# Kernel optimization log

Hardware: AMD Instinct MI355X
Metric: run time of the kernel (lower is better)

## Reference

```python
import jax, jax.numpy as jnp
import numpy as np

# dims chosen per input_specs / init_kwargs
B, S, D_IN, UNITS, WIN = 4, 2048, 512, 64, 32
W = 2 * WIN + 1  # max window length


def setup_inputs() -> dict:
    key = jax.random.key(0)
    ks = jax.random.split(key, 8)
    p = lambda k, shape: jax.random.normal(k, shape, dtype=jnp.float32) * 0.02
    return {
        "query": jax.random.normal(ks[0], (B, S, D_IN), dtype=jnp.float32),
        "value": jax.random.normal(ks[1], (B, S, D_IN), dtype=jnp.float32),
        "Wq": p(ks[2], (D_IN, UNITS)), "bq": jnp.zeros((UNITS,), jnp.float32),
        "Wk": p(ks[3], (D_IN, UNITS)), "bk": jnp.zeros((UNITS,), jnp.float32),
        "Wv": p(ks[4], (D_IN, UNITS)), "bv": jnp.zeros((UNITS,), jnp.float32),
    }


def reference(query, value, Wq, bq, Wk, bk, Wv, bv):
    # Dense projections (query stream -> Q, value stream -> K and V)
    Q = query @ Wq + bq
    K = value @ Wk + bk
    V = value @ Wv + bv

    i = np.arange(S)
    start = np.maximum(i - WIN, 0)            # [S]
    end = np.minimum(i + WIN + 1, S)          # [S]
    lengths = end - start                      # [S] window length per position
    offsets = np.concatenate([[0], np.cumsum(lengths)[:-1]])
    L = int(lengths.sum())                     # total output seq length (concat of all windows)

    idx = start[:, None] + np.arange(W)[None, :]   # [S, W] window token indices
    valid = idx < end[:, None]                      # [S, W] which slots exist
    idx_c = np.minimum(idx, S - 1)                  # clamp for safe gather

    idx_c = jnp.asarray(idx_c)
    valid_j = jnp.asarray(valid)

    # Gather overlapping windows: [B, S, W, UNITS]
    Ql = Q[:, idx_c]
    Kl = K[:, idx_c]
    Vl = V[:, idx_c]

    # Faithful to original: ALL window rows act as queries for window i.
    scale = 1.0 / jnp.sqrt(jnp.asarray(UNITS, dtype=Q.dtype))
    scores = jnp.einsum("bswd,bsud->bswu", Ql, Kl) * scale  # [B, S, W, W]
    neg = jnp.finfo(scores.dtype).min
    scores = jnp.where(valid_j[None, :, None, :], scores, neg)  # mask padded keys
    weights = jax.nn.softmax(scores, axis=-1)
    out_local = jnp.einsum("bswu,bsud->bswd", weights, Vl)  # [B, S, W, UNITS]

    # Concat valid rows of every window along seq axis -> [B, L, UNITS]
    flat_pos = jnp.asarray(offsets)[:, None] + jnp.arange(W)[None, :]  # [S, W]
    flat_pos = jnp.where(valid_j, flat_pos, L)  # invalid rows dumped in slot L
    out = jnp.zeros((Q.shape[0], L + 1, UNITS), dtype=out_local.dtype)
    out = out.at[:, flat_pos.reshape(-1)].set(out_local.reshape(Q.shape[0], -1, UNITS))
    return out[:, :L]
```

## Files before the change

kernel.cpp:

```cpp
#include <hip/hip_runtime.h>
#include <hip/hip_bf16.h>

#define BB 4
#define SS 2048
#define DIN 512
#define UU 64
#define WINR 32
#define LTOT 132064
#define GQ 16
#define NWP 144
#define KST 66

typedef __attribute__((ext_vector_type(8))) short short8;
typedef __attribute__((ext_vector_type(4))) float float4v;

static __device__ __forceinline__ ushort f2bf(float f) {
    union { __hip_bfloat16 h; ushort u; } c;
    c.h = __float2bfloat16(f);
    return c.u;
}
static __device__ __forceinline__ float bf2f(ushort u) {
    union { float f; uint v; } c;
    c.v = ((uint)u) << 16;
    return c.f;
}

__device__ __forceinline__ int offs_of(int s) {
    int a = s < (SS - 33) ? s : (SS - 33);
    int m = (s - 33) > 0 ? (s - 33) : 0;
    return a * (a - 1) / 2 + 33 * a + (s - a) * SS - m * (m + 1) / 2;
}

__global__ __launch_bounds__(256) void prep_w(
    const float* __restrict__ Wq, const float* __restrict__ Wk, const float* __restrict__ Wv,
    ushort* __restrict__ Wt)
{
    __shared__ float T[64][65];
    const int mtx = blockIdx.x >> 3;
    const int kc  = blockIdx.x & 7;
    const float* W = (mtx == 0) ? Wq : ((mtx == 1) ? Wk : Wv);
    const int tid = threadIdx.x;
    for (int idx = tid; idx < 64 * 64; idx += 256) {
        const int k = idx >> 6, n = idx & 63;
        T[n][k] = W[(size_t)(kc * 64 + k) * UU + n];
    }
    __syncthreads();
    for (int idx = tid; idx < 64 * 64; idx += 256) {
        const int n = idx >> 6, kl = idx & 63;
        Wt[(size_t)mtx * UU * DIN + (size_t)n * DIN + kc * 64 + kl] = f2bf(T[n][kl]);
    }
}

__global__ __launch_bounds__(256) void qkv_mfma(
    const float* __restrict__ query, const float* __restrict__ value,
    const ushort* __restrict__ Wt,
    const float* __restrict__ bq, const float* __restrict__ bk, const float* __restrict__ bv,
    float* __restrict__ Qs, ushort* __restrict__ Kf, ushort* __restrict__ Vf)
{
    __shared__ float red[4][16 * UU];
    const int bid = blockIdx.x;
    const int mtx = bid >> 9;
    const int rt  = bid & 511;
    const int tid = threadIdx.x;
    const int kq = tid >> 6;
    const int lane = tid & 63;
    const int m16 = lane & 15, quad = lane >> 4;

    const float* X = (mtx == 0) ? query : value;
    const float* Xrow = X + (size_t)(rt * 16 + m16) * DIN + kq * 128 + quad * 8;
    const ushort* Wm = Wt + (size_t)mtx * UU * DIN + (size_t)m16 * DIN + kq * 128 + quad * 8;

    float4v acc[4];
#pragma unroll
    for (int nb = 0; nb < 4; ++nb) acc[nb] = (float4v){0.f, 0.f, 0.f, 0.f};

#pragma unroll
    for (int kk = 0; kk < 4; ++kk) {
        const float4 xa = *(const float4*)(Xrow + kk * 32);
        const float4 xb = *(const float4*)(Xrow + kk * 32 + 4);
        short8 a;
        a[0] = (short)f2bf(xa.x); a[1] = (short)f2bf(xa.y);
        a[2] = (short)f2bf(xa.z); a[3] = (short)f2bf(xa.w);
        a[4] = (short)f2bf(xb.x); a[5] = (short)f2bf(xb.y);
        a[6] = (short)f2bf(xb.z); a[7] = (short)f2bf(xb.w);
#pragma unroll
        for (int nb = 0; nb < 4; ++nb) {
            const short8 bfr = *(const short8*)(Wm + (size_t)nb * 16 * DIN + kk * 32);
            acc[nb] = __builtin_amdgcn_mfma_f32_16x16x32_bf16(a, bfr, acc[nb], 0, 0, 0);
        }
    }

#pragma unroll
    for (int nb = 0; nb < 4; ++nb)
#pragma unroll
        for (int reg = 0; reg < 4; ++reg)
            red[kq][(quad * 4 + reg) * UU + nb * 16 + m16] = acc[nb][reg];
    __syncthreads();

    const float* bias = (mtx == 0) ? bq : ((mtx == 1) ? bk : bv);
#pragma unroll
    for (int i = 0; i < 4; ++i) {
        const int e = tid + 256 * i;
        const int col = e & 63, row = e >> 6;
        float s = red[0][e] + red[1][e] + red[2][e] + red[3][e] + bias[col];
        const size_t gi = (size_t)(rt * 16 + row) * UU + col;
        if (mtx == 0)      Qs[gi] = s * 0.125f;
        else if (mtx == 1) Kf[gi] = f2bf(s);
        else               Vf[gi] = f2bf(s);
    }
}

__global__ __launch_bounds__(1024) void attn_kernel(
    const float* __restrict__ Qs, const ushort* __restrict__ Kf,
    const ushort* __restrict__ Vf, float* __restrict__ out)
{
    __shared__ ushort Kl[NWP * KST];
    __shared__ ushort Vl[NWP * KST];
    __shared__ float  ev[GQ][NWP];
    __shared__ float  qr[GQ][UU];

    const int blk = blockIdx.x;
    const int b = blk >> 7;
    const int q0 = (blk & 127) << 4;
    const int tid = threadIdx.x;

    const int j0 = max(q0 - 2 * WINR, 0);
    const int j1 = min(q0 + GQ - 1 + 2 * WINR + 1, SS);
    const int nw = j1 - j0;

    if (tid < GQ * UU)
        qr[tid >> 6][tid & 63] = Qs[((size_t)b * SS + q0) * UU + tid];

    const uint* Kg = (const uint*)(Kf + ((size_t)b * SS + j0) * UU);
    const uint* Vg = (const uint*)(Vf + ((size_t)b * SS + j0) * UU);
    for (int idx = tid; idx < nw * 32; idx += 1024) {
        const int j = idx >> 5, d2 = idx & 31;
        ((uint*)(Kl + j * KST))[d2] = Kg[idx];
        ((uint*)(Vl + j * KST))[d2] = Vg[idx];
    }
    __syncthreads();

    for (int item = tid; item < GQ * NWP; item += 1024) {
        const int g = item / NWP, jj = item - g * NWP;
        float e = 0.f;
        if (jj < nw) {
            const uint* kr = (const uint*)(Kl + jj * KST);
            const float* q = qr[g];
            float dot = 0.f;
#pragma unroll
            for (int p = 0; p < UU / 2; ++p) {
                const uint kp = kr[p];
                dot = fmaf(q[2 * p],     bf2f((ushort)kp),         dot);
                dot = fmaf(q[2 * p + 1], bf2f((ushort)(kp >> 16)), dot);
            }
            e = __expf(dot);
        }
        ev[g][jj] = e;
    }
    __syncthreads();

    const int w = tid >> 6, lane = tid & 63;
    const int qi = q0 + w;
    const int s_lo = max(qi - WINR, 0);
    const int s_hi = min(qi + WINR, SS - 1);
    int st = max(s_lo - WINR, 0);
    int en = min(s_lo + WINR + 1, SS);
    const float* evg = ev[w];

    float acc = 0.f, den = 0.f;
    for (int j = st; j < en; ++j) {
        const float e = evg[j - j0];
        acc = fmaf(e, bf2f(Vl[(j - j0) * KST + lane]), acc);
        den += e;
    }
    int off = offs_of(s_lo);
    float* outb = out + (size_t)b * LTOT * UU;
    for (int s = s_lo;; ++s) {
        outb[(size_t)(off + qi - st) * UU + lane] = acc * __builtin_amdgcn_rcpf(den);
        if (s == s_hi) break;
        off += en - st;
        if (en < SS) {
            const float e = evg[en - j0];
            acc = fmaf(e, bf2f(Vl[(en - j0) * KST + lane]), acc);
            den += e;
            ++en;
        }
        if (s + 1 > WINR) {
            const float e = evg[st - j0];
            acc = fmaf(-e, bf2f(Vl[(st - j0) * KST + lane]), acc);
            den -= e;
            ++st;
        }
    }
}

extern "C" void kernel_launch(void* const* d_in, const int* in_sizes, int n_in,
                              void* d_out, int out_size, void* d_ws, size_t ws_size,
                              hipStream_t stream) {
    const float* query = (const float*)d_in[0];
    const float* value = (const float*)d_in[1];
    const float* Wq = (const float*)d_in[2];
    const float* bq = (const float*)d_in[3];
    const float* Wk = (const float*)d_in[4];
    const float* bk = (const float*)d_in[5];
    const float* Wv = (const float*)d_in[6];
    const float* bv = (const float*)d_in[7];
    float* out = (float*)d_out;

    float* Qs = (float*)d_ws;
    ushort* Kf = (ushort*)(Qs + (size_t)BB * SS * UU);
    ushort* Vf = Kf + (size_t)BB * SS * UU;
    ushort* Wt = (ushort*)((float*)d_out + (size_t)out_size) - (size_t)3 * UU * DIN;

    prep_w<<<24, 256, 0, stream>>>(Wq, Wk, Wv, Wt);
    qkv_mfma<<<3 * 512, 256, 0, stream>>>(query, value, Wt, bq, bk, bv, Qs, Kf, Vf);
    attn_kernel<<<512, 1024, 0, stream>>>(Qs, Kf, Vf, out);
}
```

Before: 210.5 us.

## Transpose V in LDS, compute per-query scores from global K, vectorize sliding window

The attention kernel now stores V transposed and zero-padded in LDS, so each lane reads contiguous V values with 128-bit loads. K is no longer staged: each wavefront computes scores for its own query straight from global K, masking non-window keys to zero. The running window sum is split into separate add and remove accumulators processed eight at a time with vector loads. This cuts LDS traffic and scalar per-step loads, but adds redundant global K reads and an extra zeroing pass, and subtracting the two accumulators may change float rounding.

```diff
diff --git a/kernel.cpp b/kernel.cpp
--- a/kernel.cpp
+++ b/kernel.cpp
@@ -8,11 +8,11 @@
 #define WINR 32
 #define LTOT 132064
 #define GQ 16
-#define NWP 144
-#define KST 66
+#define VST 200
 
 typedef __attribute__((ext_vector_type(8))) short short8;
 typedef __attribute__((ext_vector_type(4))) float float4v;
+typedef __attribute__((ext_vector_type(4))) uint uint4v;
 
 static __device__ __forceinline__ ushort f2bf(float f) {
     union { __hip_bfloat16 h; ushort u; } c;
@@ -22,6 +22,11 @@
 static __device__ __forceinline__ float bf2f(ushort u) {
     union { float f; uint v; } c;
     c.v = ((uint)u) << 16;
+    return c.f;
+}
+static __device__ __forceinline__ float bfbits(uint u) {
+    union { float f; uint v; } c;
+    c.v = u;
     return c.f;
 }
 
@@ -114,83 +119,133 @@
     const float* __restrict__ Qs, const ushort* __restrict__ Kf,
     const ushort* __restrict__ Vf, float* __restrict__ out)
 {
-    __shared__ ushort Kl[NWP * KST];
-    __shared__ ushort Vl[NWP * KST];
-    __shared__ float  ev[GQ][NWP];
-    __shared__ float  qr[GQ][UU];
+    __shared__ ushort Vt[UU * VST];
+    __shared__ float  evf[GQ * VST];
 
     const int blk = blockIdx.x;
     const int b = blk >> 7;
     const int q0 = (blk & 127) << 4;
     const int tid = threadIdx.x;
+    const int lane = tid & 63;
+    const int wq = __builtin_amdgcn_readfirstlane(tid >> 6);
 
     const int j0 = max(q0 - 2 * WINR, 0);
     const int j1 = min(q0 + GQ - 1 + 2 * WINR + 1, SS);
     const int nw = j1 - j0;
 
-    if (tid < GQ * UU)
-        qr[tid >> 6][tid & 63] = Qs[((size_t)b * SS + q0) * UU + tid];
-
-    const uint* Kg = (const uint*)(Kf + ((size_t)b * SS + j0) * UU);
+    for (int idx = tid; idx < UU * VST / 2; idx += 1024) ((uint*)Vt)[idx] = 0u;
+    if (tid < GQ * 40) evf[(tid / 40) * VST + (tid % 40)] = 0.f;
+    __syncthreads();
+
     const uint* Vg = (const uint*)(Vf + ((size_t)b * SS + j0) * UU);
     for (int idx = tid; idx < nw * 32; idx += 1024) {
         const int j = idx >> 5, d2 = idx & 31;
-        ((uint*)(Kl + j * KST))[d2] = Kg[idx];
-        ((uint*)(Vl + j * KST))[d2] = Vg[idx];
-    }
-    __syncthreads();
-
-    for (int item = tid; item < GQ * NWP; item += 1024) {
-        const int g = item / NWP, jj = item - g * NWP;
-        float e = 0.f;
-        if (jj < nw) {
-            const uint* kr = (const uint*)(Kl + jj * KST);
-            const float* q = qr[g];
-            float dot = 0.f;
-#pragma unroll
-            for (int p = 0; p < UU / 2; ++p) {
-                const uint kp = kr[p];
-                dot = fmaf(q[2 * p],     bf2f((ushort)kp),         dot);
-                dot = fmaf(q[2 * p + 1], bf2f((ushort)(kp >> 16)), dot);
-            }
-            e = __expf(dot);
-        }
-        ev[g][jj] = e;
-    }
-    __syncthreads();
-
-    const int w = tid >> 6, lane = tid & 63;
-    const int qi = q0 + w;
+        const uint v = Vg[idx];
+        Vt[(2 * d2) * VST + 40 + j]     = (ushort)v;
+        Vt[(2 * d2 + 1) * VST + 40 + j] = (ushort)(v >> 16);
+    }
+    __syncthreads();
+
+    const int qi = q0 + wq;
+    const int blo = max(qi - 2 * WINR, 0);
+    const int bhi = min(qi + 2 * WINR + 1, SS);
+    const float* qp = Qs + ((size_t)b * SS + qi) * UU;
+#pragma unroll
+    for (int pass = 0; pass < 3; ++pass) {
+        const int jj = pass * 64 + lane;
+        const int j = j0 + jj;
+        const bool live = (jj < nw) && (j >= blo) && (j < bhi);
+        const uint* kr = (const uint*)(Kf + ((size_t)b * SS + (live ? j : j0)) * UU);
+        float dot = 0.f;
+#pragma unroll
+        for (int c = 0; c < 8; ++c) {
+            const uint4v kp = *(const uint4v*)(kr + c * 4);
+#pragma unroll
+            for (int u = 0; u < 4; ++u) {
+                dot = fmaf(qp[c * 8 + 2 * u],     bfbits(kp[u] << 16),         dot);
+                dot = fmaf(qp[c * 8 + 2 * u + 1], bfbits(kp[u] & 0xffff0000u), dot);
+            }
+        }
+        const float e = live ? __expf(dot) : 0.f;
+        if (jj < VST - 40) evf[wq * VST + 40 + jj] = e;
+    }
+    __syncthreads();
+
     const int s_lo = max(qi - WINR, 0);
     const int s_hi = min(qi + WINR, SS - 1);
-    int st = max(s_lo - WINR, 0);
-    int en = min(s_lo + WINR + 1, SS);
-    const float* evg = ev[w];
-
-    float acc = 0.f, den = 0.f;
-    for (int j = st; j < en; ++j) {
-        const float e = evg[j - j0];
-        acc = fmaf(e, bf2f(Vl[(j - j0) * KST + lane]), acc);
-        den += e;
-    }
+    const int a = (s_lo - j0 - 7) & 7;
+    const int s_start = s_lo - a;
+    const int I_s = s_start - j0 + 8;
+    const int I_f = I_s - 7;
+    const int A0 = I_f + 72;
+
+    const ushort* vrow = Vt + lane * VST;
+    const float*  erow = evf + wq * VST;
+
+    float accA = 0.f, denA = 0.f, accR = 0.f, denR = 0.f;
+#pragma unroll
+    for (int t = 0; t < 9; ++t) {
+        const int base = I_f + 8 * t;
+        const uint4v  vv = *(const uint4v*)(vrow + base);
+        const float4v e0 = *(const float4v*)(erow + base);
+        const float4v e1 = *(const float4v*)(erow + base + 4);
+#pragma unroll
+        for (int k = 0; k < 8; ++k) {
+            const float e = (k < 4) ? e0[k] : e1[k - 4];
+            const uint wv = vv[k >> 1];
+            const float v = (k & 1) ? bfbits(wv & 0xffff0000u) : bfbits(wv << 16);
+            accA = fmaf(e, v, accA);
+            denA += e;
+        }
+    }
+
+    float pE7 = erow[I_s];
+    float pV7 = bf2f(vrow[I_s]);
+
     int off = offs_of(s_lo);
     float* outb = out + (size_t)b * LTOT * UU;
-    for (int s = s_lo;; ++s) {
-        outb[(size_t)(off + qi - st) * UU + lane] = acc * __builtin_amdgcn_rcpf(den);
-        if (s == s_hi) break;
-        off += en - st;
-        if (en < SS) {
-            const float e = evg[en - j0];
-            acc = fmaf(e, bf2f(Vl[(en - j0) * KST + lane]), acc);
-            den += e;
-            ++en;
-        }
-        if (s + 1 > WINR) {
-            const float e = evg[st - j0];
-            acc = fmaf(-e, bf2f(Vl[(st - j0) * KST + lane]), acc);
-            den -= e;
-            ++st;
-        }
+    const int ng = (s_hi - s_start + 8) >> 3;
+    for (int g = 0; g < ng; ++g) {
+        const int Ab = A0 + 8 * g;
+        const uint4v  Av  = *(const uint4v*)(vrow + Ab);
+        const float4v Ae0 = *(const float4v*)(erow + Ab);
+        const float4v Ae1 = *(const float4v*)(erow + Ab + 4);
+        const int Rb = I_f + 8 * (g + 1);
+        const uint4v  Rv  = *(const uint4v*)(vrow + Rb);
+        const float4v Re0 = *(const float4v*)(erow + Rb);
+        const float4v Re1 = *(const float4v*)(erow + Rb + 4);
+        int s = s_start + 8 * g;
+#pragma unroll
+        for (int k = 0; k < 8; ++k, ++s) {
+            if (s >= s_lo && s <= s_hi) {
+                const int st = (s - WINR > 0) ? s - WINR : 0;
+                const int en = (s + WINR + 1 < SS) ? s + WINR + 1 : SS;
+                const float r = __builtin_amdgcn_rcpf(denA - denR);
+                outb[(size_t)(off + qi - st) * UU + lane] = (accA - accR) * r;
+                off += en - st;
+            }
+            {
+                const float e = (k < 4) ? Ae0[k] : Ae1[k - 4];
+                const uint wv = Av[k >> 1];
+                const float v = (k & 1) ? bfbits(wv & 0xffff0000u) : bfbits(wv << 16);
+                accA = fmaf(e, v, accA);
+                denA += e;
+            }
+            {
+                float e, v;
+                if (k == 0) { e = pE7; v = pV7; }
+                else {
+                    const int m = k - 1;
+                    e = (m < 4) ? Re0[m] : Re1[m - 4];
+                    const uint wv = Rv[m >> 1];
+                    v = (m & 1) ? bfbits(wv & 0xffff0000u) : bfbits(wv << 16);
+                }
+                accR = fmaf(e, v, accR);
+                denR += e;
+            }
+        }
+        pE7 = Re1[3];
+        pV7 = bfbits(Rv[3] & 0xffff0000u);
     }
 }
 
```

Result: slower. 215.4 us (+2.3%).
